# Kernel optimization log

Measured on AMD Instinct MI355X. Metric: run time of the kernel, lower is better.

## Reference

```python
import jax, jax.numpy as jnp
from jax import lax
import numpy as np

NEG = jnp.float32(-1e9)


def monotonic_alignment_search(logp, text_lengths, mel_lengths):
    """Glow-TTS style MAS. logp: [B, Tt, Tm] (log_softmax over text axis).
    Returns integer durations [B, Tt] summing to mel_lengths per batch."""
    B, Tt, Tm = logp.shape
    i_range = jnp.arange(Tt)
    text_mask = i_range[None, :] < text_lengths[:, None]            # [B, Tt]
    logp = jnp.where(text_mask[:, :, None], logp, NEG)

    # ---- forward DP over mel frames: Q[i,j] = logp[i,j] + max(Q[i,j-1], Q[i-1,j-1])
    q0 = jnp.where(i_range[None, :] == 0, logp[:, :, 0], NEG)        # [B, Tt]

    def fwd(q, lp_j):
        q_shift = jnp.concatenate([jnp.full((B, 1), NEG), q[:, :-1]], axis=1)
        take_diag = q_shift > q                                      # came from i-1
        q_new = lp_j + jnp.maximum(q, q_shift)
        return q_new, take_diag

    _, choices = lax.scan(fwd, q0, jnp.moveaxis(logp[:, :, 1:], 2, 0))  # [Tm-1, B, Tt]
    choices = jnp.concatenate([jnp.zeros((1, B, Tt), bool), choices], axis=0)  # align j

    # ---- backtrack from (text_len-1, mel_len-1) down to j=0
    b_idx = jnp.arange(B)

    def bwd(i, j):
        active = j < mel_lengths                                     # [B]
        dur_inc = (active[:, None] & (i_range[None, :] == i[:, None]))
        ch = choices[j, b_idx, i]                                    # [B] bool
        i_new = jnp.where(active & (j > 0), i - ch.astype(i.dtype), i)
        return i_new, dur_inc

    i0 = text_lengths - 1
    _, durs = lax.scan(bwd, i0, jnp.arange(Tm - 1, -1, -1))
    return durs.sum(0).astype(jnp.int32)                             # [B, Tt]


def length_regulate(h_text, durations, mel_lengths, Tm):
    """Expand h_text [B,Tt,D] by durations [B,Tt] to [B,Tm,D]."""
    B, Tt, D = h_text.shape
    cum = jnp.cumsum(durations, axis=1)                              # [B, Tt]
    j = jnp.arange(Tm)
    idx = (cum[:, None, :] <= j[None, :, None]).sum(-1)              # [B, Tm]
    idx = jnp.clip(idx, 0, Tt - 1)
    h_exp = jnp.take_along_axis(h_text, idx[:, :, None], axis=1)     # [B, Tm, D]
    mel_mask = j[None, :] < mel_lengths[:, None]
    return h_exp * mel_mask[:, :, None].astype(h_exp.dtype)


def setup_inputs() -> dict:
    B, Tt, Tm, D, M = 32, 512, 2048, 512, 80
    k = jax.random.split(jax.random.key(0), 6)
    return {
        "h_text": jax.random.normal(k[0], (B, Tt, D), jnp.float32),
        "mel": jax.random.normal(k[1], (B, M, Tm), jnp.float32),
        "text_lengths": jax.random.randint(k[2], (B,), 256, Tt + 1, jnp.int32),
        "mel_lengths": jax.random.randint(k[3], (B,), 1024, Tm + 1, jnp.int32),
        "w_proj": jax.random.normal(k[4], (D, M), jnp.float32) * 0.02,
        "b_proj": jnp.zeros((D,), jnp.float32),
        "log_dur_pred": jax.random.normal(k[5], (B, Tt), jnp.float32) * 0.5,
    }


def reference(h_text, mel, text_lengths, mel_lengths, w_proj, b_proj, log_dur_pred):
    B, Tt, D = h_text.shape
    Tm = mel.shape[2]

    # mel_proj = Linear(n_mels -> d_model) on mel.transpose(1,2)
    mel_proj = jnp.einsum('bmt,dm->btd', mel, w_proj) + b_proj       # [B, Tm, D]

    # alignment scores + masked log_softmax over text axis
    attn = jnp.einsum('btd,bsd->bts', h_text, mel_proj)              # [B, Tt, Tm]
    text_mask = jnp.arange(Tt)[None, :] >= text_lengths[:, None]
    mel_mask = jnp.arange(Tm)[None, :] >= mel_lengths[:, None]
    attn = jnp.where(text_mask[:, :, None], NEG, attn)
    attn = jnp.where(mel_mask[:, None, :], NEG, attn)
    logp = jax.nn.log_softmax(attn, axis=1)

    durations = monotonic_alignment_search(logp, text_lengths, mel_lengths)

    # duration loss (masked sum-MSE in log domain)
    dur_mask = (jnp.arange(Tt)[None, :] < text_lengths[:, None]).astype(jnp.float32)
    log_dur_gt = jnp.log(jnp.clip(durations.astype(jnp.float32), 1.0, None))
    diff = log_dur_pred * dur_mask - log_dur_gt * dur_mask
    dur_loss = jnp.sum(diff * diff) / jnp.sum(dur_mask)

    h_expanded = length_regulate(h_text, durations, mel_lengths, Tm)  # [B, Tm, D]
    return (h_expanded, dur_loss, durations)
```

## Files before the change

kernel.cpp:

```cpp
#include <hip/hip_runtime.h>
#include <math.h>

#define Bn 32
#define TT 512
#define TM 2048
#define DD 512
#define MMp 80
#define NEGF (-1.0e9f)

constexpr size_t LOSS_OFF = (size_t)Bn * TM * DD;
constexpr size_t DUR_OFF  = LOSS_OFF + 1;

__global__ __launch_bounds__(256) void k0_wtx(const float* __restrict__ w,
                                              const float* __restrict__ bias,
                                              float* __restrict__ wTx) {
    int m = blockIdx.x;
    for (int d = threadIdx.x; d < DD; d += 256) {
        float v = 0.f;
        if (m < 80) v = w[d * 80 + m];
        else if (m == 80) v = bias[d];
        wTx[m * DD + d] = v;
    }
}

__global__ __launch_bounds__(256) void k1_hw(const float* __restrict__ h_text,
                                             const float* __restrict__ wTx,
                                             float* __restrict__ hwX) {
    int bid = blockIdx.x;
    int b = bid >> 3;
    int i0 = (bid & 7) * 64;
    int t = threadIdx.x;
    int tr = t & 15, tc = t >> 4;
    __shared__ __align__(16) float Asub[64 * 68];
    __shared__ __align__(16) float Bsub[96 * 68];
    float acc[4][6];
#pragma unroll
    for (int a = 0; a < 4; ++a)
#pragma unroll
        for (int c = 0; c < 6; ++c) acc[a][c] = 0.f;

    for (int d0 = 0; d0 < DD; d0 += 64) {
        __syncthreads();
#pragma unroll
        for (int p = 0; p < 4; ++p) {
            int lin = p * 256 + t;
            int r = lin >> 4, dq = lin & 15;
            *(float4*)&Asub[r * 68 + dq * 4] =
                *(const float4*)&h_text[((size_t)(b * TT + i0 + r)) * DD + d0 + dq * 4];
        }
#pragma unroll
        for (int p = 0; p < 6; ++p) {
            int lin = p * 256 + t;
            int cc = lin >> 4, dq = lin & 15;
            *(float4*)&Bsub[cc * 68 + dq * 4] =
                *(const float4*)&wTx[(size_t)cc * DD + d0 + dq * 4];
        }
        __syncthreads();
#pragma unroll
        for (int dd = 0; dd < 16; ++dd) {
            float4 a[4], bb[6];
#pragma unroll
            for (int ri = 0; ri < 4; ++ri)
                a[ri] = *(const float4*)&Asub[(tr * 4 + ri) * 68 + dd * 4];
#pragma unroll
            for (int ci = 0; ci < 6; ++ci)
                bb[ci] = *(const float4*)&Bsub[(tc * 6 + ci) * 68 + dd * 4];
#pragma unroll
            for (int ri = 0; ri < 4; ++ri)
#pragma unroll
                for (int ci = 0; ci < 6; ++ci) {
                    acc[ri][ci] += a[ri].x * bb[ci].x;
                    acc[ri][ci] += a[ri].y * bb[ci].y;
                    acc[ri][ci] += a[ri].z * bb[ci].z;
                    acc[ri][ci] += a[ri].w * bb[ci].w;
                }
        }
    }
#pragma unroll
    for (int ri = 0; ri < 4; ++ri)
#pragma unroll
        for (int ci = 0; ci < 6; ++ci)
            hwX[((size_t)b * 96 + tc * 6 + ci) * DD + i0 + tr * 4 + ri] = acc[ri][ci];
}

__global__ __launch_bounds__(256) void k2_attn(const float* __restrict__ hwX,
                                               const float* __restrict__ mel,
                                               const int* __restrict__ tlen,
                                               const int* __restrict__ mlen,
                                               float* __restrict__ logpT) {
    const int b = blockIdx.y;
    const int ml = mlen[b];
    const int j0 = blockIdx.x * 32;
    if (j0 >= ml) return;
    const int tl = tlen[b];
    const int tid = threadIdx.x;
    const int ig = tid >> 2;
    const int jg = tid & 3;

    __shared__ __align__(16) float hwS[16 * 512];
    __shared__ __align__(16) float melS[16 * 32];
    __shared__ float red[32 * 64];
    __shared__ float colmax[32];
    __shared__ float lsum[32];

    float acc[8][8];
#pragma unroll
    for (int a = 0; a < 8; ++a)
#pragma unroll
        for (int c = 0; c < 8; ++c) acc[a][c] = 0.f;

    for (int mc = 0; mc < 80; mc += 16) {
        __syncthreads();
#pragma unroll
        for (int p = 0; p < 8; ++p) {
            int lin = p * 256 + tid;
            int mm = lin >> 7, iq = lin & 127;
            *(float4*)&hwS[mm * 512 + iq * 4] =
                *(const float4*)&hwX[((size_t)b * 96 + mc + mm) * DD + iq * 4];
        }
#pragma unroll
        for (int p = 0; p < 2; ++p) {
            int lin = p * 256 + tid;
            int mm = lin >> 5, jj = lin & 31;
            melS[lin] = mel[((size_t)b * 80 + mc + mm) * TM + j0 + jj];
        }
        __syncthreads();
#pragma unroll
        for (int mm = 0; mm < 16; ++mm) {
            float4 a0 = *(const float4*)&hwS[mm * 512 + ig * 8];
            float4 a1 = *(const float4*)&hwS[mm * 512 + ig * 8 + 4];
            float4 b0 = *(const float4*)&melS[mm * 32 + jg * 8];
            float4 b1 = *(const float4*)&melS[mm * 32 + jg * 8 + 4];
            float av[8] = {a0.x, a0.y, a0.z, a0.w, a1.x, a1.y, a1.z, a1.w};
            float bv[8] = {b0.x, b0.y, b0.z, b0.w, b1.x, b1.y, b1.z, b1.w};
#pragma unroll
            for (int ii = 0; ii < 8; ++ii)
#pragma unroll
                for (int jj = 0; jj < 8; ++jj) acc[ii][jj] += av[ii] * bv[jj];
        }
    }
    float4 h0 = *(const float4*)&hwX[((size_t)b * 96 + 80) * DD + ig * 8];
    float4 h1 = *(const float4*)&hwX[((size_t)b * 96 + 80) * DD + ig * 8 + 4];
    float hb[8] = {h0.x, h0.y, h0.z, h0.w, h1.x, h1.y, h1.z, h1.w};
#pragma unroll
    for (int ii = 0; ii < 8; ++ii) {
        bool valid = (ig * 8 + ii) < tl;
#pragma unroll
        for (int jj = 0; jj < 8; ++jj)
            acc[ii][jj] = valid ? (acc[ii][jj] + hb[ii]) : NEGF;
    }
    __syncthreads();
#pragma unroll
    for (int jj = 0; jj < 8; ++jj) {
        float m = acc[0][jj];
#pragma unroll
        for (int ii = 1; ii < 8; ++ii) m = fmaxf(m, acc[ii][jj]);
        red[(jg * 8 + jj) * 64 + ig] = m;
    }
    __syncthreads();
    if (tid < 32) {
        float m = red[tid * 64];
        for (int g = 1; g < 64; ++g) m = fmaxf(m, red[tid * 64 + g]);
        colmax[tid] = m;
    }
    __syncthreads();
#pragma unroll
    for (int jj = 0; jj < 8; ++jj) {
        float cm = colmax[jg * 8 + jj];
        float s = 0.f;
#pragma unroll
        for (int ii = 0; ii < 8; ++ii) s += expf(acc[ii][jj] - cm);
        red[(jg * 8 + jj) * 64 + ig] = s;
    }
    __syncthreads();
    if (tid < 32) {
        float s = 0.f;
        for (int g = 0; g < 64; ++g) s += red[tid * 64 + g];
        lsum[tid] = logf(s);
    }
    __syncthreads();
#pragma unroll
    for (int jj = 0; jj < 8; ++jj) {
        int j = j0 + jg * 8 + jj;
        if (j < ml) {
            float cm = colmax[jg * 8 + jj], ls = lsum[jg * 8 + jj];
            float o[8];
#pragma unroll
            for (int ii = 0; ii < 8; ++ii) {
                int i = ig * 8 + ii;
                o[ii] = (i < tl) ? ((acc[ii][jj] - cm) - ls) : NEGF;
            }
            float* dst = &logpT[((size_t)b * TM + j) * TT + ig * 8];
            *(float4*)dst = make_float4(o[0], o[1], o[2], o[3]);
            *(float4*)(dst + 4) = make_float4(o[4], o[5], o[6], o[7]);
        }
    }
}

#define CH 8
#define NSLOT 3
#define NCHUNK 256

#define WAITLGKM asm volatile("s_waitcnt lgkmcnt(0)" ::: "memory")

__device__ __forceinline__ float dpp_shr1(float old, float src) {
    return __int_as_float(__builtin_amdgcn_update_dpp(
        __float_as_int(old), __float_as_int(src), 0x138, 0xF, 0xF, false));
}

__global__ __launch_bounds__(1024, 4) void k3_dp(const float* __restrict__ logpT,
                                                 const int* __restrict__ tlen,
                                                 const int* __restrict__ mlen,
                                                 unsigned* __restrict__ gwords,
                                                 int* __restrict__ idxmap,
                                                 float* __restrict__ dOut) {
    const int b = blockIdx.x;
    const int tid = threadIdx.x;
    const int wid = tid >> 6;
    const int lane = tid & 63;
    const int tl = tlen[b];
    const int ml = mlen[b];

    __shared__ __align__(16) float ring[NSLOT * CH * 512];
    __shared__ int flags[NSLOT];
    __shared__ int consumed;
    __shared__ int durs[TT];

    for (int x = tid; x < TT; x += 1024) durs[x] = 0;
    if (tid < NSLOT) flags[tid] = -1;
    if (tid == 0) consumed = 0;
    __syncthreads();

    const float* colbase = logpT + (size_t)b * TM * TT;
    unsigned* gwb = gwords + (size_t)b * TT * 64;
    volatile int* vflags = flags;
    volatile int* vcons = &consumed;

    if (wid == 0) {
        float q[8];
        unsigned accb[8];
#pragma unroll
        for (int k = 0; k < 8; ++k) { q[k] = NEGF; accb[k] = 0u; }
        if (lane == 0) q[0] = colbase[0];
        unsigned* gp = gwb + lane * 8 * 64;

        int c = 1;
        for (int g = 0; g < NCHUNK; ++g) {
            const int s = (g % NSLOT);
            while (vflags[s] != g) { }
            asm volatile("" ::: "memory");
            const float* cp = &ring[s * (CH * 512)];
            float4 la0 = *(const float4*)&cp[lane * 8];
            float4 la1 = *(const float4*)&cp[lane * 8 + 4];
            float4 lb0, lb1;
#pragma unroll
            for (int cc = 0; cc < CH; ++cc) {
                if (cc + 1 < CH) {
                    lb0 = *(const float4*)&cp[(cc + 1) * 512 + lane * 8];
                    lb1 = *(const float4*)&cp[(cc + 1) * 512 + lane * 8 + 4];
                }
                if (c < TM) {
                    float lp[8] = {la0.x, la0.y, la0.z, la0.w,
                                   la1.x, la1.y, la1.z, la1.w};
                    float nb[8];
                    nb[0] = dpp_shr1(NEGF, q[7]);
#pragma unroll
                    for (int k = 1; k < 8; ++k) nb[k] = q[k - 1];
                    const unsigned m32 = 1u << (c & 31);
#pragma unroll
                    for (int k = 0; k < 8; ++k) {
                        if (nb[k] > q[k]) accb[k] |= m32;
                        q[k] = lp[k] + fmaxf(q[k], nb[k]);
                    }
                    if ((c & 31) == 31) {
#pragma unroll
                        for (int k = 0; k < 8; ++k) { gp[k * 64] = accb[k]; accb[k] = 0u; }
                        gp += 1;
                    }
                    ++c;
                }
                la0 = lb0; la1 = lb1;
            }
            asm volatile("" ::: "memory");
            *vcons = g + 1;
        }
    } else {
        const int pp = wid - 1;
        for (int g = pp; g < NCHUNK; g += 15) {
            const int cbase = 1 + g * CH;
            float4 va[CH], vb[CH];
#pragma unroll
            for (int cc = 0; cc < CH; ++cc) {
                int cx = cbase + cc;
                cx = (cx > TM - 1) ? (TM - 1) : cx;
                const float4* gsrc = (const float4*)(colbase + (size_t)cx * 512) + lane * 2;
                va[cc] = gsrc[0];
                vb[cc] = gsrc[1];
            }
            if (g >= NSLOT) {
                while (*vcons < g - (NSLOT - 1)) __builtin_amdgcn_s_sleep(2);
                asm volatile("" ::: "memory");
            }
            const int s = (g % NSLOT);
            float* dst = &ring[s * (CH * 512)];
#pragma unroll
            for (int cc = 0; cc < CH; ++cc) {
                *(float4*)&dst[cc * 512 + lane * 8]     = va[cc];
                *(float4*)&dst[cc * 512 + lane * 8 + 4] = vb[cc];
            }
            WAITLGKM;
            vflags[s] = g;
        }
    }
    __threadfence();
    __syncthreads();

    if (wid == 0) {
        int i = tl - 1;
        int j = ml - 1;
        unsigned r0, r1, r2, r3, r4, r5, r6, r7;
        {
            int a0 = tl - 1, a1 = tl - 2, a2 = tl - 3, a3 = tl - 4;
            int a4 = tl - 5, a5 = tl - 6, a6 = tl - 7, a7 = tl - 8;
            a1 = a1 < 0 ? 0 : a1; a2 = a2 < 0 ? 0 : a2; a3 = a3 < 0 ? 0 : a3;
            a4 = a4 < 0 ? 0 : a4; a5 = a5 < 0 ? 0 : a5; a6 = a6 < 0 ? 0 : a6;
            a7 = a7 < 0 ? 0 : a7;
            r0 = gwb[a0 * 64 + lane]; r1 = gwb[a1 * 64 + lane];
            r2 = gwb[a2 * 64 + lane]; r3 = gwb[a3 * 64 + lane];
            r4 = gwb[a4 * 64 + lane]; r5 = gwb[a5 * 64 + lane];
            r6 = gwb[a6 * 64 + lane]; r7 = gwb[a7 * 64 + lane];
        }
        int nf = tl - 9;
        int guard = TT + 2;
        while (guard-- > 0) {
            unsigned w = r0;
            r0 = r1; r1 = r2; r2 = r3; r3 = r4; r4 = r5; r5 = r6; r6 = r7;
            {
                int rf = (nf < 0) ? 0 : nf;
                r7 = gwb[rf * 64 + lane];
                --nf;
            }
            int jw = j >> 5, rr = j & 31;
            unsigned topmask = (rr == 31) ? 0xFFFFFFFFu : ((1u << (rr + 1)) - 1u);
            unsigned wm = (lane < jw) ? w : ((lane == jw) ? (w & topmask) : 0u);
            unsigned long long bal = __ballot(wm != 0u);
            if (bal == 0ull) {
                if (lane == 0) durs[i] = j + 1;
                break;
            }
            int hl = 63 - __clzll(bal);
            unsigned whl = (unsigned)__builtin_amdgcn_readlane((int)wm, hl);
            int jp = (hl << 5) + (31 - __clz(whl));
            if (lane == 0) durs[i] = j - jp + 1;
            j = jp - 1;
            if (--i < 0) break;
        }
    }
    __syncthreads();

    if (wid == 0) {
        int d[8], pre[8];
        int run = 0;
#pragma unroll
        for (int k = 0; k < 8; ++k) { d[k] = durs[lane * 8 + k]; pre[k] = run; run += d[k]; }
        int v = run;
#pragma unroll
        for (int off = 1; off < 64; off <<= 1) {
            int n = __shfl_up(v, off);
            if (lane >= off) v += n;
        }
        int base = v - run;
#pragma unroll
        for (int k = 0; k < 8; ++k) {
            int i = lane * 8 + k;
            dOut[DUR_OFF + (size_t)b * TT + i] = (float)d[k];
            int st = base + pre[k];
            for (int t2 = 0; t2 < d[k]; ++t2) idxmap[b * TM + st + t2] = i;
        }
    }
}

__global__ __launch_bounds__(128) void k4_expand(const float* __restrict__ h_text,
                                                 const int* __restrict__ idxmap,
                                                 const int* __restrict__ mlen,
                                                 float* __restrict__ dOut) {
    int bid = blockIdx.x;
    int b = bid >> 11;
    int j = bid & (TM - 1);
    int t = threadIdx.x;
    float4* orow = (float4*)dOut + (size_t)bid * 128;
    if (j < mlen[b]) {
        int i = idxmap[bid];
        const float4* hrow = (const float4*)h_text + ((size_t)(b * TT + i)) * 128;
        orow[t] = hrow[t];
    } else {
        orow[t] = make_float4(0.f, 0.f, 0.f, 0.f);
    }
}

__global__ __launch_bounds__(256) void k5_loss(const float* __restrict__ pred,
                                               const int* __restrict__ tlen,
                                               float* __restrict__ dOut) {
    __shared__ float rs[256];
    __shared__ int rc[256];
    int t = threadIdx.x;
    float s = 0.f;
    int c = 0;
    for (int idx = t; idx < Bn * TT; idx += 256) {
        int b = idx >> 9, i = idx & 511;
        if (i < tlen[b]) {
            float dv = dOut[DUR_OFF + idx];
            float lg = logf(fmaxf(dv, 1.0f));
            float df = pred[idx] - lg;
            s += df * df;
            c += 1;
        }
    }
    rs[t] = s; rc[t] = c;
    __syncthreads();
    for (int off = 128; off > 0; off >>= 1) {
        if (t < off) { rs[t] += rs[t + off]; rc[t] += rc[t + off]; }
        __syncthreads();
    }
    if (t == 0) dOut[LOSS_OFF] = rs[0] / (float)rc[0];
}

extern "C" void kernel_launch(void* const* d_in, const int* in_sizes, int n_in,
                              void* d_out, int out_size, void* d_ws, size_t ws_size,
                              hipStream_t stream) {
    const float* h_text = (const float*)d_in[0];
    const float* mel    = (const float*)d_in[1];
    const int*   tlen   = (const int*)d_in[2];
    const int*   mlen   = (const int*)d_in[3];
    const float* w      = (const float*)d_in[4];
    const float* bias   = (const float*)d_in[5];
    const float* pred   = (const float*)d_in[6];
    float* out = (float*)d_out;

    float*    logpT  = (float*)d_ws;
    float*    hwX    = logpT + (size_t)Bn * TM * TT;
    float*    wTx    = hwX + (size_t)Bn * 96 * DD;
    unsigned* gwords = (unsigned*)(wTx + 96 * DD);
    int*      idxmap = (int*)(gwords + (size_t)Bn * TT * 64);

    k0_wtx<<<dim3(96), dim3(256), 0, stream>>>(w, bias, wTx);
    k1_hw<<<dim3(256), dim3(256), 0, stream>>>(h_text, wTx, hwX);
    k2_attn<<<dim3(64, 32), dim3(256), 0, stream>>>(hwX, mel, tlen, mlen, logpT);
    k3_dp<<<dim3(32), dim3(1024), 0, stream>>>(logpT, tlen, mlen, gwords, idxmap, out);
    k4_expand<<<dim3(Bn * TM), dim3(128), 0, stream>>>(h_text, idxmap, mlen, out);
    k5_loss<<<dim3(1), dim3(256), 0, stream>>>(pred, tlen, out);
}
```

Baseline: 879.8 us.

## Feed the DP ring buffer with direct global-to-LDS loads from fewer producer waves

The producer waves of the serial alignment DP kernel now copy logp columns into the shared ring with global_load_lds (16 bytes per lane) instead of loading into registers and then storing to LDS. The block shrinks from 1024 to 512 threads, leaving 7 producer waves. The ring changes from 3 slots of 8 columns to 5 slots of 6 columns. The DP step is rewritten as a macro over scalar registers and updates lanes from the top index down. The goal is to lower the producer's register and VALU cost and keep the single DP wave fed, though producers now wait for a free slot before issuing their loads.

```diff
diff --git a/kernel.cpp b/kernel.cpp
--- a/kernel.cpp
+++ b/kernel.cpp
@@ -197,23 +197,49 @@
     }
 }
 
-#define CH 8
-#define NSLOT 3
-#define NCHUNK 256
-
-#define WAITLGKM asm volatile("s_waitcnt lgkmcnt(0)" ::: "memory")
+#define CH 6
+#define NSLOT 5
+#define NCHUNK 342
+
+#define WAITALL  asm volatile("s_waitcnt vmcnt(0)" ::: "memory")
+
+__device__ __forceinline__ void lds_dma16(const float* g, float* l) {
+    __builtin_amdgcn_global_load_lds((const __attribute__((address_space(1))) void*)g,
+                                     (__attribute__((address_space(3))) void*)l,
+                                     16, 0, 0);
+}
 
 __device__ __forceinline__ float dpp_shr1(float old, float src) {
     return __int_as_float(__builtin_amdgcn_update_dpp(
         __float_as_int(old), __float_as_int(src), 0x138, 0xF, 0xF, false));
 }
 
-__global__ __launch_bounds__(1024, 4) void k3_dp(const float* __restrict__ logpT,
-                                                 const int* __restrict__ tlen,
-                                                 const int* __restrict__ mlen,
-                                                 unsigned* __restrict__ gwords,
-                                                 int* __restrict__ idxmap,
-                                                 float* __restrict__ dOut) {
+#define DPSTEP(V0,V1,V2,V3,V4,V5,V6,V7)                                   \
+    do {                                                                  \
+        float n0 = dpp_shr1(NEGF, q7);                                    \
+        unsigned m32 = 1u << (c & 31);                                    \
+        if (q6 > q7) a7 |= m32;  q7 = (V7) + fmaxf(q7, q6);               \
+        if (q5 > q6) a6 |= m32;  q6 = (V6) + fmaxf(q6, q5);               \
+        if (q4 > q5) a5 |= m32;  q5 = (V5) + fmaxf(q5, q4);               \
+        if (q3 > q4) a4 |= m32;  q4 = (V4) + fmaxf(q4, q3);               \
+        if (q2 > q3) a3 |= m32;  q3 = (V3) + fmaxf(q3, q2);               \
+        if (q1 > q2) a2 |= m32;  q2 = (V2) + fmaxf(q2, q1);               \
+        if (q0 > q1) a1 |= m32;  q1 = (V1) + fmaxf(q1, q0);               \
+        if (n0 > q0) a0 |= m32;  q0 = (V0) + fmaxf(q0, n0);               \
+        if ((c & 31) == 31) {                                             \
+            gp[0]   = a0; gp[64]  = a1; gp[128] = a2; gp[192] = a3;       \
+            gp[256] = a4; gp[320] = a5; gp[384] = a6; gp[448] = a7;       \
+            a0 = a1 = a2 = a3 = a4 = a5 = a6 = a7 = 0u;                   \
+            gp += 1;                                                      \
+        }                                                                 \
+    } while (0)
+
+__global__ __launch_bounds__(512, 2) void k3_dp(const float* __restrict__ logpT,
+                                                const int* __restrict__ tlen,
+                                                const int* __restrict__ mlen,
+                                                unsigned* __restrict__ gwords,
+                                                int* __restrict__ idxmap,
+                                                float* __restrict__ dOut) {
     const int b = blockIdx.x;
     const int tid = threadIdx.x;
     const int wid = tid >> 6;
@@ -226,7 +252,7 @@
     __shared__ int consumed;
     __shared__ int durs[TT];
 
-    for (int x = tid; x < TT; x += 1024) durs[x] = 0;
+    for (int x = tid; x < TT; x += 512) durs[x] = 0;
     if (tid < NSLOT) flags[tid] = -1;
     if (tid == 0) consumed = 0;
     __syncthreads();
@@ -237,78 +263,56 @@
     volatile int* vcons = &consumed;
 
     if (wid == 0) {
-        float q[8];
-        unsigned accb[8];
-#pragma unroll
-        for (int k = 0; k < 8; ++k) { q[k] = NEGF; accb[k] = 0u; }
-        if (lane == 0) q[0] = colbase[0];
+        float q0 = NEGF, q1 = NEGF, q2 = NEGF, q3 = NEGF;
+        float q4 = NEGF, q5 = NEGF, q6 = NEGF, q7 = NEGF;
+        unsigned a0 = 0u, a1 = 0u, a2 = 0u, a3 = 0u;
+        unsigned a4 = 0u, a5 = 0u, a6 = 0u, a7 = 0u;
+        if (lane == 0) q0 = colbase[0];
         unsigned* gp = gwb + lane * 8 * 64;
 
         int c = 1;
         for (int g = 0; g < NCHUNK; ++g) {
-            const int s = (g % NSLOT);
+            const int s = g % NSLOT;
             while (vflags[s] != g) { }
             asm volatile("" ::: "memory");
             const float* cp = &ring[s * (CH * 512)];
             float4 la0 = *(const float4*)&cp[lane * 8];
             float4 la1 = *(const float4*)&cp[lane * 8 + 4];
-            float4 lb0, lb1;
 #pragma unroll
             for (int cc = 0; cc < CH; ++cc) {
+                float4 nx0 = la0, nx1 = la1;
                 if (cc + 1 < CH) {
-                    lb0 = *(const float4*)&cp[(cc + 1) * 512 + lane * 8];
-                    lb1 = *(const float4*)&cp[(cc + 1) * 512 + lane * 8 + 4];
+                    nx0 = *(const float4*)&cp[(cc + 1) * 512 + lane * 8];
+                    nx1 = *(const float4*)&cp[(cc + 1) * 512 + lane * 8 + 4];
                 }
                 if (c < TM) {
-                    float lp[8] = {la0.x, la0.y, la0.z, la0.w,
-                                   la1.x, la1.y, la1.z, la1.w};
-                    float nb[8];
-                    nb[0] = dpp_shr1(NEGF, q[7]);
-#pragma unroll
-                    for (int k = 1; k < 8; ++k) nb[k] = q[k - 1];
-                    const unsigned m32 = 1u << (c & 31);
-#pragma unroll
-                    for (int k = 0; k < 8; ++k) {
-                        if (nb[k] > q[k]) accb[k] |= m32;
-                        q[k] = lp[k] + fmaxf(q[k], nb[k]);
-                    }
-                    if ((c & 31) == 31) {
-#pragma unroll
-                        for (int k = 0; k < 8; ++k) { gp[k * 64] = accb[k]; accb[k] = 0u; }
-                        gp += 1;
-                    }
+                    DPSTEP(la0.x, la0.y, la0.z, la0.w, la1.x, la1.y, la1.z, la1.w);
                     ++c;
                 }
-                la0 = lb0; la1 = lb1;
+                la0 = nx0; la1 = nx1;
             }
             asm volatile("" ::: "memory");
             *vcons = g + 1;
         }
     } else {
         const int pp = wid - 1;
-        for (int g = pp; g < NCHUNK; g += 15) {
+        for (int g = pp; g < NCHUNK; g += 7) {
+            if (g >= NSLOT) {
+                while (*vcons < g - (NSLOT - 1)) __builtin_amdgcn_s_sleep(2);
+                asm volatile("" ::: "memory");
+            }
+            const int s = g % NSLOT;
+            float* dst = &ring[s * (CH * 512)];
             const int cbase = 1 + g * CH;
-            float4 va[CH], vb[CH];
 #pragma unroll
             for (int cc = 0; cc < CH; ++cc) {
                 int cx = cbase + cc;
                 cx = (cx > TM - 1) ? (TM - 1) : cx;
-                const float4* gsrc = (const float4*)(colbase + (size_t)cx * 512) + lane * 2;
-                va[cc] = gsrc[0];
-                vb[cc] = gsrc[1];
-            }
-            if (g >= NSLOT) {
-                while (*vcons < g - (NSLOT - 1)) __builtin_amdgcn_s_sleep(2);
-                asm volatile("" ::: "memory");
-            }
-            const int s = (g % NSLOT);
-            float* dst = &ring[s * (CH * 512)];
-#pragma unroll
-            for (int cc = 0; cc < CH; ++cc) {
-                *(float4*)&dst[cc * 512 + lane * 8]     = va[cc];
-                *(float4*)&dst[cc * 512 + lane * 8 + 4] = vb[cc];
-            }
-            WAITLGKM;
+                const float* gsrc = colbase + (size_t)cx * 512 + lane * 4;
+                lds_dma16(gsrc,       dst + cc * 512);
+                lds_dma16(gsrc + 256, dst + cc * 512 + 256);
+            }
+            WAITALL;
             vflags[s] = g;
         }
     }
@@ -320,15 +324,15 @@
         int j = ml - 1;
         unsigned r0, r1, r2, r3, r4, r5, r6, r7;
         {
-            int a0 = tl - 1, a1 = tl - 2, a2 = tl - 3, a3 = tl - 4;
-            int a4 = tl - 5, a5 = tl - 6, a6 = tl - 7, a7 = tl - 8;
-            a1 = a1 < 0 ? 0 : a1; a2 = a2 < 0 ? 0 : a2; a3 = a3 < 0 ? 0 : a3;
-            a4 = a4 < 0 ? 0 : a4; a5 = a5 < 0 ? 0 : a5; a6 = a6 < 0 ? 0 : a6;
-            a7 = a7 < 0 ? 0 : a7;
-            r0 = gwb[a0 * 64 + lane]; r1 = gwb[a1 * 64 + lane];
-            r2 = gwb[a2 * 64 + lane]; r3 = gwb[a3 * 64 + lane];
-            r4 = gwb[a4 * 64 + lane]; r5 = gwb[a5 * 64 + lane];
-            r6 = gwb[a6 * 64 + lane]; r7 = gwb[a7 * 64 + lane];
+            int b0 = tl - 1, b1 = tl - 2, b2 = tl - 3, b3 = tl - 4;
+            int b4 = tl - 5, b5 = tl - 6, b6 = tl - 7, b7 = tl - 8;
+            b1 = b1 < 0 ? 0 : b1; b2 = b2 < 0 ? 0 : b2; b3 = b3 < 0 ? 0 : b3;
+            b4 = b4 < 0 ? 0 : b4; b5 = b5 < 0 ? 0 : b5; b6 = b6 < 0 ? 0 : b6;
+            b7 = b7 < 0 ? 0 : b7;
+            r0 = gwb[b0 * 64 + lane]; r1 = gwb[b1 * 64 + lane];
+            r2 = gwb[b2 * 64 + lane]; r3 = gwb[b3 * 64 + lane];
+            r4 = gwb[b4 * 64 + lane]; r5 = gwb[b5 * 64 + lane];
+            r6 = gwb[b6 * 64 + lane]; r7 = gwb[b7 * 64 + lane];
         }
         int nf = tl - 9;
         int guard = TT + 2;
@@ -446,7 +450,7 @@
     k0_wtx<<<dim3(96), dim3(256), 0, stream>>>(w, bias, wTx);
     k1_hw<<<dim3(256), dim3(256), 0, stream>>>(h_text, wTx, hwX);
     k2_attn<<<dim3(64, 32), dim3(256), 0, stream>>>(hwX, mel, tlen, mlen, logpT);
-    k3_dp<<<dim3(32), dim3(1024), 0, stream>>>(logpT, tlen, mlen, gwords, idxmap, out);
+    k3_dp<<<dim3(32), dim3(512), 0, stream>>>(logpT, tlen, mlen, gwords, idxmap, out);
     k4_expand<<<dim3(Bn * TM), dim3(128), 0, stream>>>(h_text, idxmap, mlen, out);
     k5_loss<<<dim3(1), dim3(256), 0, stream>>>(pred, tlen, out);
 }
```

Result: faster. 844.9 us (-4.0%).
